# Performance work log

Measured on AMD Instinct MI355X. Metric: run time of the kernel, lower is better.

Reference implementation:

```python
import jax, jax.numpy as jnp
import numpy as np


def setup_inputs() -> dict:
    key = jax.random.key(0)
    k1, k2 = jax.random.split(key)
    B, C, H, W = 4, 64, 256, 512
    right_input = jax.random.normal(k1, (B, C, H, W), dtype=jnp.float32)
    disparity_samples = jax.random.uniform(k2, (B, 1, H, W), dtype=jnp.float32)
    return {"right_input": right_input, "disparity_samples": disparity_samples}


def reference(right_input, disparity_samples):
    B, C, H, W = right_input.shape
    dt = right_input.dtype
    # left pixel x-coordinates along width, broadcast over B,1,H
    left_y = jnp.arange(W, dtype=dt).reshape(1, 1, 1, W)
    right_y = left_y + disparity_samples                      # [B,1,H,W]
    ry_a = jnp.floor(right_y)
    ry_b = ry_a + 1.0
    wa = ry_b - right_y                                       # [B,1,H,W]
    wb = right_y - ry_a
    idx_a = jnp.clip(ry_a, 0, W - 1).astype(jnp.int32)
    idx_b = jnp.clip(ry_b, 0, W - 1).astype(jnp.int32)
    # broadcast indices across channels and gather along width (dim=3)
    idx_a = jnp.broadcast_to(idx_a, (B, C, H, W))
    idx_b = jnp.broadcast_to(idx_b, (B, C, H, W))
    feat_a = jnp.take_along_axis(right_input, idx_a, axis=3)
    feat_b = jnp.take_along_axis(right_input, idx_b, axis=3)
    warped = wa * feat_a + wb * feat_b                        # weights broadcast over C
    # zero out samples whose (unclamped) coordinate fell outside [0, W-1]
    oob = (right_y < 0).astype(dt) + (right_y > (W - 1)).astype(dt)
    return (1.0 - oob) * warped
```

## Files before the change

kernel.cpp:

```cpp
#include <hip/hip_runtime.h>

constexpr int B = 4;
constexpr int C = 64;
constexpr int H = 256;
constexpr int W = 512;
constexpr int CPB = 16;
constexpr long long HW = (long long)H * W;

__global__ __launch_bounds__(512) void spatial_warp_kernel(
    const float* __restrict__ input,
    const float* __restrict__ disp,
    float* __restrict__ out)
{
    const int w    = threadIdx.x;
    const int cg   = blockIdx.x & (C / CPB - 1);
    const int rest = blockIdx.x >> 2;
    const int h    = rest & (H - 1);
    const int b    = rest >> 8;

    const long long pix = ((long long)b * H + h) * (long long)W;

    const float d   = disp[pix + w];
    const float ry  = (float)w + d;
    const float ra  = floorf(ry);
    const float wa  = ra + 1.0f - ry;
    const float wb  = ry - ra;
    const float msk = (ry >= 0.0f && ry <= (float)(W - 1)) ? 1.0f : 0.0f;
    const float iaf = fminf(fmaxf(ra, 0.0f), (float)(W - 1));
    const int   ia  = (int)iaf;
    const bool  hi  = (ia >= W - 1);
    const int   i0  = hi ? (W - 2) : ia;
    const float waf = hi ? 0.0f : msk * wa;
    const float wbf = hi ? msk  : msk * wb;

    const int c0 = cg * CPB;
    const float* p = input + (((long long)b * C + c0) * H + h) * (long long)W;
    float*       q = out   + (((long long)b * C + c0) * H + h) * (long long)W + w;

    float va[CPB], vb[CPB];
#pragma unroll
    for (int cc = 0; cc < CPB; ++cc) {
        const float* row = p + (long long)cc * HW;
        va[cc] = row[i0];
        vb[cc] = row[i0 + 1];
    }
#pragma unroll
    for (int cc = 0; cc < CPB; ++cc) {
        __builtin_nontemporal_store(waf * va[cc] + wbf * vb[cc],
                                    q + (long long)cc * HW);
    }
}

extern "C" void kernel_launch(void* const* d_in, const int* in_sizes, int n_in,
                              void* d_out, int out_size, void* d_ws, size_t ws_size,
                              hipStream_t stream) {
    const float* input = (const float*)d_in[0];
    const float* disp  = (const float*)d_in[1];
    float* outp = (float*)d_out;

    const int grid = B * H * (C / CPB);
    spatial_warp_kernel<<<grid, 512, 0, stream>>>(input, disp, outp);
}
```

Before: 240.2 us.

## Stage input rows in LDS per wavefront and gather from shared memory

```diff
diff --git a/kernel.cpp b/kernel.cpp
--- a/kernel.cpp
+++ b/kernel.cpp
@@ -5,49 +5,81 @@
 constexpr int H = 256;
 constexpr int W = 512;
 constexpr int CPB = 16;
+constexpr int CPW = 4;
 constexpr long long HW = (long long)H * W;
 
-__global__ __launch_bounds__(512) void spatial_warp_kernel(
+__global__ __launch_bounds__(256) void spatial_warp_kernel(
     const float* __restrict__ input,
     const float* __restrict__ disp,
     float* __restrict__ out)
 {
-    const int w    = threadIdx.x;
-    const int cg   = blockIdx.x & (C / CPB - 1);
+    __shared__ float s_buf[4][2][W];
+
+    const int t    = threadIdx.x;
+    const int lane = t & 63;
+    const int wid  = t >> 6;
+
+    const int cg   = blockIdx.x & 3;
     const int rest = blockIdx.x >> 2;
     const int h    = rest & (H - 1);
     const int b    = rest >> 8;
 
-    const long long pix = ((long long)b * H + h) * (long long)W;
+    const long long pix    = ((long long)b * H + h) * (long long)W;
+    const long long rowoff = (long long)h * W;
+    const int c0 = cg * CPB + wid * CPW;
 
-    const float d   = disp[pix + w];
-    const float ry  = (float)w + d;
-    const float ra  = floorf(ry);
-    const float wa  = ra + 1.0f - ry;
-    const float wb  = ry - ra;
-    const float msk = (ry >= 0.0f && ry <= (float)(W - 1)) ? 1.0f : 0.0f;
-    const float iaf = fminf(fmaxf(ra, 0.0f), (float)(W - 1));
-    const int   ia  = (int)iaf;
-    const bool  hi  = (ia >= W - 1);
-    const int   i0  = hi ? (W - 2) : ia;
-    const float waf = hi ? 0.0f : msk * wa;
-    const float wbf = hi ? msk  : msk * wb;
+    const float* p0 = input + ((long long)(b * C + c0)) * HW + rowoff;
+    float*       q0 = out   + ((long long)(b * C + c0)) * HW + rowoff;
 
-    const int c0 = cg * CPB;
-    const float* p = input + (((long long)b * C + c0) * H + h) * (long long)W;
-    float*       q = out   + (((long long)b * C + c0) * H + h) * (long long)W + w;
+    const float* drow = disp + pix;
+    float dv[8];
+#pragma unroll
+    for (int j = 0; j < 8; ++j) dv[j] = drow[lane + 64 * j];
 
-    float va[CPB], vb[CPB];
+    float4 va[CPW], vb[CPW];
 #pragma unroll
-    for (int cc = 0; cc < CPB; ++cc) {
-        const float* row = p + (long long)cc * HW;
-        va[cc] = row[i0];
-        vb[cc] = row[i0 + 1];
+    for (int k = 0; k < CPW; ++k) {
+        const float4* rp = reinterpret_cast<const float4*>(p0 + (long long)k * HW);
+        va[k] = rp[lane];
+        vb[k] = rp[64 + lane];
     }
+    __builtin_amdgcn_sched_barrier(0);
+
+    float waf[8], wbf[8];
+    int   addr0[8];
 #pragma unroll
-    for (int cc = 0; cc < CPB; ++cc) {
-        __builtin_nontemporal_store(waf * va[cc] + wbf * vb[cc],
-                                    q + (long long)cc * HW);
+    for (int j = 0; j < 8; ++j) {
+        const int w     = lane + 64 * j;
+        const float ry  = (float)w + dv[j];
+        const float ra  = floorf(ry);
+        const float wa  = ra + 1.0f - ry;
+        const float wb  = ry - ra;
+        const float msk = (ry >= 0.0f && ry <= (float)(W - 1)) ? 1.0f : 0.0f;
+        const float iaf = fminf(fmaxf(ra, 0.0f), (float)(W - 1));
+        const int   ia  = (int)iaf;
+        const bool  hi  = (ia >= W - 1);
+        const int   i0  = hi ? (W - 2) : ia;
+        waf[j]   = hi ? 0.0f : msk * wa;
+        wbf[j]   = hi ? msk  : msk * wb;
+        addr0[j] = i0 * 4;
+    }
+
+#pragma unroll
+    for (int k = 0; k < CPW; ++k) {
+        float* buf = &s_buf[wid][k & 1][0];
+        reinterpret_cast<float4*>(buf)[lane]      = va[k];
+        reinterpret_cast<float4*>(buf)[64 + lane] = vb[k];
+        asm volatile("s_waitcnt lgkmcnt(0)" ::: "memory");
+        __builtin_amdgcn_sched_barrier(0);
+
+        float* op = q0 + (long long)k * HW;
+        const char* bufc = reinterpret_cast<const char*>(buf);
+#pragma unroll
+        for (int j = 0; j < 8; ++j) {
+            const float fa = *reinterpret_cast<const float*>(bufc + addr0[j]);
+            const float fb = *reinterpret_cast<const float*>(bufc + addr0[j] + 4);
+            op[lane + 64 * j] = waf[j] * fa + wbf[j] * fb;
+        }
     }
 }
 
@@ -59,5 +91,5 @@
     float* outp = (float*)d_out;
 
     const int grid = B * H * (C / CPB);
-    spatial_warp_kernel<<<grid, 512, 0, stream>>>(input, disp, outp);
+    spatial_warp_kernel<<<grid, 256, 0, stream>>>(input, disp, outp);
 }
```

Result: no change. 241.3 us (+0.5%).

## Stage input rows into LDS via async global_load_lds with double buffering

Applied to the files above, without the earlier changes.

```diff
diff --git a/kernel.cpp b/kernel.cpp
--- a/kernel.cpp
+++ b/kernel.cpp
@@ -1,53 +1,92 @@
 #include <hip/hip_runtime.h>
+#include <stdint.h>
 
 constexpr int B = 4;
 constexpr int C = 64;
 constexpr int H = 256;
 constexpr int W = 512;
-constexpr int CPB = 16;
+constexpr int RPW = 16;
 constexpr long long HW = (long long)H * W;
 
-__global__ __launch_bounds__(512) void spatial_warp_kernel(
+template<int K>
+__device__ __forceinline__ void vwait() {
+    asm volatile("s_waitcnt vmcnt(%0)" :: "i"(K) : "memory");
+    __builtin_amdgcn_sched_barrier(0);
+}
+
+__device__ __forceinline__ void stage_row(const float* gsrc, float* ldst, int lane) {
+    __builtin_amdgcn_global_load_lds(
+        (const __attribute__((address_space(1))) void*)(gsrc + lane * 4),
+        (__attribute__((address_space(3))) void*)(ldst),
+        16, 0, 0);
+    __builtin_amdgcn_global_load_lds(
+        (const __attribute__((address_space(1))) void*)(gsrc + 256 + lane * 4),
+        (__attribute__((address_space(3))) void*)(ldst + 256),
+        16, 0, 0);
+}
+
+__global__ __launch_bounds__(256) void spatial_warp_kernel(
     const float* __restrict__ input,
     const float* __restrict__ disp,
     float* __restrict__ out)
 {
-    const int w    = threadIdx.x;
-    const int cg   = blockIdx.x & (C / CPB - 1);
-    const int rest = blockIdx.x >> 2;
-    const int h    = rest & (H - 1);
-    const int b    = rest >> 8;
+    __shared__ float s_in[4][2][W];
+    __shared__ float s_dp[4][2][W];
 
-    const long long pix = ((long long)b * H + h) * (long long)W;
+    const int t    = threadIdx.x;
+    const int lane = t & 63;
+    const int wid  = t >> 6;
 
-    const float d   = disp[pix + w];
-    const float ry  = (float)w + d;
-    const float ra  = floorf(ry);
-    const float wa  = ra + 1.0f - ry;
-    const float wb  = ry - ra;
-    const float msk = (ry >= 0.0f && ry <= (float)(W - 1)) ? 1.0f : 0.0f;
-    const float iaf = fminf(fmaxf(ra, 0.0f), (float)(W - 1));
-    const int   ia  = (int)iaf;
-    const bool  hi  = (ia >= W - 1);
-    const int   i0  = hi ? (W - 2) : ia;
-    const float waf = hi ? 0.0f : msk * wa;
-    const float wbf = hi ? msk  : msk * wb;
+    const int hr = blockIdx.x & 15;
+    const int cq = (blockIdx.x >> 4) & 15;
+    const int b  = blockIdx.x >> 8;
+    const int c  = cq * 4 + wid;
+    const int h0 = hr * RPW;
 
-    const int c0 = cg * CPB;
-    const float* p = input + (((long long)b * C + c0) * H + h) * (long long)W;
-    float*       q = out   + (((long long)b * C + c0) * H + h) * (long long)W + w;
+    const float* gin  = input + ((long long)(b * C + c)) * HW + (long long)h0 * W;
+    const float* gdp  = disp  + ((long long)b * H + h0) * (long long)W;
+    float*       gout = out   + ((long long)(b * C + c)) * HW + (long long)h0 * W;
 
-    float va[CPB], vb[CPB];
+    stage_row(gin,     &s_in[wid][0][0], lane);
+    stage_row(gdp,     &s_dp[wid][0][0], lane);
+    stage_row(gin + W, &s_in[wid][1][0], lane);
+    stage_row(gdp + W, &s_dp[wid][1][0], lane);
+
 #pragma unroll
-    for (int cc = 0; cc < CPB; ++cc) {
-        const float* row = p + (long long)cc * HW;
-        va[cc] = row[i0];
-        vb[cc] = row[i0 + 1];
-    }
+    for (int r = 0; r < RPW; ++r) {
+        if (r == 0)            vwait<4>();
+        else if (r == RPW - 1) vwait<8>();
+        else                   vwait<12>();
+
+        const float* si   = &s_in[wid][r & 1][0];
+        const float* sd   = &s_dp[wid][r & 1][0];
+        float*       orow = gout + (long long)r * W;
+
 #pragma unroll
-    for (int cc = 0; cc < CPB; ++cc) {
-        __builtin_nontemporal_store(waf * va[cc] + wbf * vb[cc],
-                                    q + (long long)cc * HW);
+        for (int j = 0; j < 8; ++j) {
+            const int   w   = lane + 64 * j;
+            const float d   = sd[w];
+            const float ry  = (float)w + d;
+            const float ra  = floorf(ry);
+            const float wa  = ra + 1.0f - ry;
+            const float wb  = ry - ra;
+            const float msk = (ry >= 0.0f && ry <= (float)(W - 1)) ? 1.0f : 0.0f;
+            const float iaf = fminf(fmaxf(ra, 0.0f), (float)(W - 1));
+            const int   ia  = (int)iaf;
+            const bool  hi  = (ia >= W - 1);
+            const int   i0  = hi ? (W - 2) : ia;
+            const float waf = hi ? 0.0f : msk * wa;
+            const float wbf = hi ? msk  : msk * wb;
+            const float fa  = si[i0];
+            const float fb  = si[i0 + 1];
+            __builtin_nontemporal_store(waf * fa + wbf * fb, orow + w);
+        }
+
+        if (r + 2 < RPW) {
+            __builtin_amdgcn_sched_barrier(0);
+            stage_row(gin + (long long)(r + 2) * W, &s_in[wid][r & 1][0], lane);
+            stage_row(gdp + (long long)(r + 2) * W, &s_dp[wid][r & 1][0], lane);
+        }
     }
 }
 
@@ -58,6 +97,6 @@
     const float* disp  = (const float*)d_in[1];
     float* outp = (float*)d_out;
 
-    const int grid = B * H * (C / CPB);
-    spatial_warp_kernel<<<grid, 512, 0, stream>>>(input, disp, outp);
+    const int grid = B * (C / 4) * (H / RPW);
+    spatial_warp_kernel<<<grid, 256, 0, stream>>>(input, disp, outp);
 }
```

Result: no change. 236.0 us (-1.8%).
